# Kernel optimization log

Hardware: AMD Instinct MI355X
Metric: run time of the kernel (lower is better)

## Reference

```python
import jax, jax.numpy as jnp
import numpy as np

B, S, C = 2, 2048, 1024
U, H = 1024, 16
FFH = int(U * 4.0)
NEG = -1e9
EPS = 1e-5


def setup_inputs() -> dict:
    key = jax.random.key(0)
    ks = jax.random.split(key, 16)
    w = lambda k, sh: jax.random.normal(k, sh, dtype=jnp.float32) * 0.02
    return {
        'x': jax.random.normal(ks[0], (B, S, C), dtype=jnp.float32),
        'wq': w(ks[1], (C, U)), 'bq': jnp.zeros((U,), jnp.float32),
        'wk': w(ks[2], (C, U)), 'bk': jnp.zeros((U,), jnp.float32),
        'wv': w(ks[3], (C, U)), 'bv': jnp.zeros((U,), jnp.float32),
        'wf1': w(ks[4], (U, FFH)), 'bf1': jnp.zeros((FFH,), jnp.float32),
        'wf2': w(ks[5], (FFH, U)), 'bf2': jnp.zeros((U,), jnp.float32),
        'ln_g': jnp.ones((S, U), jnp.float32), 'ln_b': jnp.zeros((S, U), jnp.float32),
        'ffln_g': jnp.ones((S, U), jnp.float32), 'ffln_b': jnp.zeros((S, U), jnp.float32),
    }


def _ln2d(x, g, b):
    # LayerNorm over last two dims ([len_ts, units]) as in nn.LayerNorm([S, U])
    m = jnp.mean(x, axis=(-2, -1), keepdims=True)
    v = jnp.mean(jnp.square(x - m), axis=(-2, -1), keepdims=True)
    return (x - m) * jax.lax.rsqrt(v + EPS) * g + b


def reference(x, wq, bq, wk, bk, wv, bv, wf1, bf1, wf2, bf2, ln_g, ln_b, ffln_g, ffln_b):
    dh = U // H
    Q = (x @ wq + bq).reshape(B, S, H, dh)
    K = (x @ wk + bk).reshape(B, S, H, dh)
    V = (x @ wv + bv).reshape(B, S, H, dh)
    scores = jnp.einsum('bqhd,bkhd->bhqk', Q, K) / jnp.sqrt(jnp.float32(dh))
    mask = jnp.tril(jnp.ones((S, S), dtype=bool))  # causal tril buffer
    scores = jnp.where(mask, scores, NEG)
    attn = jax.nn.softmax(scores, axis=-1)
    out = jnp.einsum('bhqk,bkhd->bqhd', attn, V).reshape(B, S, U)
    out = out + x  # residual
    out = _ln2d(out, ln_g, ln_b)
    ff = jax.nn.relu(out @ wf1 + bf1) @ wf2 + bf2
    out = _ln2d(out + ff, ffln_g, ffln_b)
    return out
```

## Files before the change

### kernel.cpp

```cpp
#include <hip/hip_runtime.h>

typedef short s16x8 __attribute__((ext_vector_type(8)));
typedef float f32x4 __attribute__((ext_vector_type(4)));
typedef unsigned short u16x4 __attribute__((ext_vector_type(4)));

#define DEV static __device__ __forceinline__

DEV unsigned short f2bf(float f) {
  union { float f; unsigned u; } v; v.f = f;
  unsigned r = v.u + 0x7FFFu + ((v.u >> 16) & 1u);
  return (unsigned short)(r >> 16);
}
DEV float bf2f(unsigned short u) {
  union { unsigned u; float f; } v; v.u = (unsigned)u << 16; return v.f;
}

#define GLDS16(src, dst) \
  __builtin_amdgcn_global_load_lds((const __attribute__((address_space(1))) void*)(src), \
                                   (__attribute__((address_space(3))) void*)(dst), 16, 0, 0)

#define MFMA(a, b, c) __builtin_amdgcn_mfma_f32_16x16x32_bf16((a), (b), (c), 0, 0, 0)

__global__ __launch_bounds__(256) void k_f32_to_bf16(const float* __restrict__ in,
                                                     unsigned short* __restrict__ out, int n4) {
  int i = blockIdx.x * 256 + threadIdx.x;
  if (i >= n4) return;
  float4 v = ((const float4*)in)[i];
  u16x4 o; o.x = f2bf(v.x); o.y = f2bf(v.y); o.z = f2bf(v.z); o.w = f2bf(v.w);
  ((u16x4*)out)[i] = o;
}

__global__ __launch_bounds__(256) void k_transpose_w(const float* __restrict__ W,
                                                     unsigned short* __restrict__ Wt,
                                                     int K, int N, float scale) {
  __shared__ float t[64][65];
  int k0 = blockIdx.x * 64, n0 = blockIdx.y * 64;
  int tid = threadIdx.x;
#pragma unroll
  for (int i = 0; i < 16; ++i) {
    int idx = tid + i * 256; int r = idx >> 6, c = idx & 63;
    t[r][c] = W[(size_t)(k0 + r) * N + (n0 + c)];
  }
  __syncthreads();
#pragma unroll
  for (int i = 0; i < 16; ++i) {
    int idx = tid + i * 256; int r = idx >> 6, c = idx & 63;
    Wt[(size_t)(n0 + r) * K + (k0 + c)] = f2bf(t[c][r] * scale);
  }
}

__global__ void k_concat3(const float* __restrict__ a, const float* __restrict__ b,
                          const float* __restrict__ c, float* __restrict__ out, int n, float sa) {
  int i = blockIdx.x * 256 + threadIdx.x;
  if (i >= 3 * n) return;
  int j = (i < n) ? i : (i < 2 * n ? i - n : i - 2 * n);
  out[i] = (i < n) ? a[j] * sa : (i < 2 * n ? b[j] : c[j]);
}

template <int MODE>
__global__ __launch_bounds__(512, 2) void k_gemm8(
    const unsigned short* __restrict__ A, int lda,
    const unsigned short* __restrict__ Bt, int ldb,
    const float* __restrict__ bias,
    unsigned short* __restrict__ Cb, float* __restrict__ Cf, int ldc,
    int K, int nnt, size_t zstride) {
  __shared__ __align__(16) unsigned short As[2 * 2 * 8192];
  __shared__ __align__(16) unsigned short Bs[2 * 2 * 8192];
  int nwg = gridDim.x;
  int bid = blockIdx.x;
  int cpx = nwg >> 3;
  int swz = (bid & 7) * cpx + (bid >> 3);
  int mt = swz / nnt, nt = swz % nnt;
  int m0 = mt * 256, n0 = nt * 256;
  int tid = threadIdx.x, w = tid >> 6, l = tid & 63;
  int wm = (w >> 2) * 128, wn = (w & 3) * 64;
  int kb = blockIdx.z * K;

  int sr = tid >> 2;
  int gsrc = (tid & 3) ^ ((sr >> 1) & 3);
  const unsigned short* Ag0 = A + (size_t)(m0 + sr) * lda + kb + gsrc * 8;
  const unsigned short* Ag1 = Ag0 + (size_t)128 * lda;
  const unsigned short* Bg0 = Bt + (size_t)(n0 + sr) * ldb + kb + gsrc * 8;
  const unsigned short* Bg1 = Bg0 + (size_t)128 * ldb;

#define STG_A(t, kh) do { int _c = (t) * 64 + (kh) * 32; int _d = ((((t) & 1) * 2 + (kh)) * 8192); \
    GLDS16(Ag0 + _c, &As[_d + tid * 8]); GLDS16(Ag1 + _c, &As[_d + 4096 + tid * 8]); } while (0)
#define STG_B(t, kh) do { int _c = (t) * 64 + (kh) * 32; int _d = ((((t) & 1) * 2 + (kh)) * 8192); \
    GLDS16(Bg0 + _c, &Bs[_d + tid * 8]); GLDS16(Bg1 + _c, &Bs[_d + 4096 + tid * 8]); } while (0)

  int lswz = (l >> 1) & 3;
  int acol = ((l >> 4) ^ lswz) * 8;
  const unsigned short* Afr = &As[(wm + (l & 15)) * 32 + acol];
  const unsigned short* Bfr = &Bs[(wn + (l & 15)) * 32 + acol];

  f32x4 acc[8][4] = {};
  int nkt = K >> 6;

  STG_A(0, 0); STG_B(0, 0); STG_A(0, 1); STG_B(0, 1); STG_A(1, 0); STG_B(1, 0);
  asm volatile("s_waitcnt vmcnt(4)" ::: "memory");
  __builtin_amdgcn_s_barrier();
  __builtin_amdgcn_sched_barrier(0);

  for (int t = 0; t < nkt; ++t) {
    int cur = t & 1, rem = nkt - t;
    const unsigned short* ab = Afr + cur * 16384;
    const unsigned short* bb = Bfr + cur * 16384;
    s16x8 af[4], bf[4];
    if (t + 1 < nkt) STG_A(t + 1, 1);
#pragma unroll
    for (int nr = 0; nr < 4; ++nr) bf[nr] = *(const s16x8*)(bb + nr * 512);
#pragma unroll
    for (int mr = 0; mr < 4; ++mr) af[mr] = *(const s16x8*)(ab + mr * 512);
    __builtin_amdgcn_s_setprio(1);
#pragma unroll
    for (int mr = 0; mr < 4; ++mr)
#pragma unroll
      for (int nr = 0; nr < 4; ++nr)
        acc[mr][nr] = MFMA(af[mr], bf[nr], acc[mr][nr]);
    __builtin_amdgcn_s_setprio(0);
    if (t + 1 < nkt) STG_B(t + 1, 1);
#pragma unroll
    for (int mr = 0; mr < 4; ++mr) af[mr] = *(const s16x8*)(ab + 2048 + mr * 512);
    __builtin_amdgcn_s_setprio(1);
#pragma unroll
    for (int mr = 0; mr < 4; ++mr)
#pragma unroll
      for (int nr = 0; nr < 4; ++nr)
        acc[mr + 4][nr] = MFMA(af[mr], bf[nr], acc[mr + 4][nr]);
    __builtin_amdgcn_s_setprio(0);
    if (rem >= 2) { asm volatile("s_waitcnt vmcnt(4)" ::: "memory"); }
    else          { asm volatile("s_waitcnt vmcnt(0)" ::: "memory"); }
    __builtin_amdgcn_s_barrier();
    __builtin_amdgcn_sched_barrier(0);
    if (t + 2 < nkt) STG_A(t + 2, 0);
#pragma unroll
    for (int nr = 0; nr < 4; ++nr) bf[nr] = *(const s16x8*)(bb + 8192 + nr * 512);
#pragma unroll
    for (int mr = 0; mr < 4; ++mr) af[mr] = *(const s16x8*)(ab + 8192 + mr * 512);
    __builtin_amdgcn_s_setprio(1);
#pragma unroll
    for (int mr = 0; mr < 4; ++mr)
#pragma unroll
      for (int nr = 0; nr < 4; ++nr)
        acc[mr][nr] = MFMA(af[mr], bf[nr], acc[mr][nr]);
    __builtin_amdgcn_s_setprio(0);
    if (t + 2 < nkt) STG_B(t + 2, 0);
#pragma unroll
    for (int mr = 0; mr < 4; ++mr) af[mr] = *(const s16x8*)(ab + 8192 + 2048 + mr * 512);
    __builtin_amdgcn_s_setprio(1);
#pragma unroll
    for (int mr = 0; mr < 4; ++mr)
#pragma unroll
      for (int nr = 0; nr < 4; ++nr)
        acc[mr + 4][nr] = MFMA(af[mr], bf[nr], acc[mr + 4][nr]);
    __builtin_amdgcn_s_setprio(0);
    if (rem >= 3) { asm volatile("s_waitcnt vmcnt(4)" ::: "memory"); }
    else          { asm volatile("s_waitcnt vmcnt(0)" ::: "memory"); }
    __builtin_amdgcn_s_barrier();
    __builtin_amdgcn_sched_barrier(0);
  }
#undef STG_A
#undef STG_B

  unsigned short* Cbz = (MODE == 3) ? (Cb + zstride * blockIdx.z) : Cb;
#pragma unroll
  for (int mr = 0; mr < 8; ++mr) {
    int rb = m0 + wm + mr * 16 + (l >> 4) * 4;
#pragma unroll
    for (int nr = 0; nr < 4; ++nr) {
      int col = n0 + wn + nr * 16 + (l & 15);
      float bv = (MODE == 3) ? 0.f : bias[col];
#pragma unroll
      for (int j = 0; j < 4; ++j) {
        float v = acc[mr][nr][j] + bv;
        size_t off = (size_t)(rb + j) * ldc + col;
        if (MODE == 1) v = fmaxf(v, 0.f);
        Cbz[off] = f2bf(v);
      }
    }
  }
}

__global__ __launch_bounds__(256) void k_ff2_reduce(
    unsigned short* __restrict__ slices, const float* __restrict__ bias,
    const unsigned short* __restrict__ resid, float* __restrict__ partials) {
  __shared__ float red[8];
  int i = blockIdx.x;
  size_t rb = (size_t)i * 4096;
  int c = threadIdx.x * 4;
  u16x4 a0 = *(const u16x4*)(slices + rb + c);
  u16x4 a1 = *(const u16x4*)(slices + rb + 1024 + c);
  u16x4 a2 = *(const u16x4*)(slices + rb + 2048 + c);
  u16x4 a3 = *(const u16x4*)(slices + rb + 3072 + c);
  float4 bv = *(const float4*)(bias + c);
  u16x4 rv = *(const u16x4*)(resid + (size_t)i * 1024 + c);
  float4 o;
  o.x = bf2f(a0.x) + bf2f(a1.x) + bf2f(a2.x) + bf2f(a3.x) + bv.x + bf2f(rv.x);
  o.y = bf2f(a0.y) + bf2f(a1.y) + bf2f(a2.y) + bf2f(a3.y) + bv.y + bf2f(rv.y);
  o.z = bf2f(a0.z) + bf2f(a1.z) + bf2f(a2.z) + bf2f(a3.z) + bv.z + bf2f(rv.z);
  o.w = bf2f(a0.w) + bf2f(a1.w) + bf2f(a2.w) + bf2f(a3.w) + bv.w + bf2f(rv.w);
  __syncthreads();
  *(float4*)((float*)slices + (size_t)i * 2048 + c) = o;
  float bsum = o.x + o.y + o.z + o.w;
  float bsq = o.x * o.x + o.y * o.y + o.z * o.z + o.w * o.w;
  int wv = threadIdx.x >> 6, lv = threadIdx.x & 63;
#pragma unroll
  for (int mk = 1; mk < 64; mk <<= 1) { bsum += __shfl_xor(bsum, mk); bsq += __shfl_xor(bsq, mk); }
  if (lv == 0) { red[wv] = bsum; red[4 + wv] = bsq; }
  __syncthreads();
  if (threadIdx.x == 0) {
    partials[i * 2] = red[0] + red[1] + red[2] + red[3];
    partials[i * 2 + 1] = red[4] + red[5] + red[6] + red[7];
  }
}

__global__ __launch_bounds__(256) void k_transpose_v(const unsigned short* __restrict__ V, int ldv,
                                                     unsigned short* __restrict__ Vt, int S, int H) {
  __shared__ __align__(16) unsigned short t[64][72];
  int s0 = blockIdx.x * 64;
  int bh = blockIdx.y; int b = bh / H, h = bh % H;
  const unsigned short* src = V + (size_t)(b * S) * ldv + h * 64;
  unsigned short* dst = Vt + (size_t)bh * 64 * S;
  int tid = threadIdx.x;
#pragma unroll
  for (int i = 0; i < 2; ++i) {
    int idx = tid + i * 256;
    int s = idx >> 3, c = (idx & 7) * 8;
    s16x8 v = *(const s16x8*)(src + (size_t)(s0 + s) * ldv + c);
#pragma unroll
    for (int j = 0; j < 8; ++j) t[c + j][s] = (unsigned short)v[j];
  }
  __syncthreads();
#pragma unroll
  for (int i = 0; i < 2; ++i) {
    int idx = tid + i * 256;
    int d = idx >> 3, c = (idx & 7) * 8;
    *(s16x8*)(dst + (size_t)d * S + s0 + c) = *(const s16x8*)&t[d][c];
  }
}

__global__ __launch_bounds__(256) void k_attn(
    const unsigned short* __restrict__ Qg, const unsigned short* __restrict__ Kg,
    const unsigned short* __restrict__ Vt, int ldqk,
    const float* __restrict__ x, float* __restrict__ hpre,
    float* __restrict__ partials, int S, int H) {
  __shared__ __align__(16) unsigned short Ks[2][64 * 64];
  __shared__ __align__(16) unsigned short Vs[2][64 * 64];
  __shared__ __align__(16) unsigned short Ps[4][16 * 64];
  __shared__ float red[8];
  int bh = blockIdx.x, b = bh >> 4, h = bh & 15;
  const int nqt = S / 64;
  int qt = nqt - 1 - (int)blockIdx.y;
  int tid = threadIdx.x, w = tid >> 6, l = tid & 63;
  const int U = H * 64;
  const unsigned short* Qb = Qg + (size_t)(b * S) * ldqk + h * 64;
  const unsigned short* Kb = Kg + (size_t)(b * S) * ldqk + h * 64;
  const unsigned short* Vb = Vt + (size_t)bh * 64 * S;
  const float* xb = x + (size_t)(b * S) * U + h * 64;
  float* hb = hpre + (size_t)(b * S) * U + h * 64;
  int sg_r[2], sg_c[2];
#pragma unroll
  for (int it = 0; it < 2; ++it) {
    int g = it * 256 + tid;
    sg_r[it] = g >> 3;
    sg_c[it] = ((g & 7) ^ ((g >> 3) & 7)) * 8;
  }
  unsigned short* Pw = &Ps[w][0];
  int qloc = l & 15;
  int kloc = (l >> 4) * 4;

  int qrow = qt * 64 + w * 16 + qloc;
  s16x8 qf0 = *(const s16x8*)(Qb + (size_t)qrow * ldqk + (l >> 4) * 8);
  s16x8 qf1 = *(const s16x8*)(Qb + (size_t)qrow * ldqk + 32 + (l >> 4) * 8);
  f32x4 o[4] = {};
  float m = -1e30f, lsum = 0.f;

#pragma unroll
  for (int it = 0; it < 2; ++it) {
    GLDS16(Kb + (size_t)sg_r[it] * ldqk + sg_c[it], &Ks[0][(it * 256 + tid) * 8]);
    GLDS16(Vb + (size_t)sg_r[it] * S + sg_c[it], &Vs[0][(it * 256 + tid) * 8]);
  }

  for (int kt = 0; kt <= qt; ++kt) {
    int cur = kt & 1;
    __syncthreads();
    if (kt < qt) {
      int nb = cur ^ 1, kn = (kt + 1) * 64;
#pragma unroll
      for (int it = 0; it < 2; ++it) {
        GLDS16(Kb + (size_t)(kn + sg_r[it]) * ldqk + sg_c[it], &Ks[nb][(it * 256 + tid) * 8]);
        GLDS16(Vb + (size_t)sg_r[it] * S + kn + sg_c[it], &Vs[nb][(it * 256 + tid) * 8]);
      }
    }
    f32x4 sc[4];
    __builtin_amdgcn_s_setprio(1);
#pragma unroll
    for (int fn = 0; fn < 4; ++fn) {
      int row = fn * 16 + (l & 15);
      s16x8 kf0 = *(const s16x8*)&Ks[cur][row * 64 + ((((l >> 4)) ^ (row & 7)) * 8)];
      s16x8 kf1 = *(const s16x8*)&Ks[cur][row * 64 + (((4 + (l >> 4)) ^ (row & 7)) * 8)];
      f32x4 z = {};
      z = MFMA(kf0, qf0, z);
      z = MFMA(kf1, qf1, z);
      sc[fn] = z;
    }
    __builtin_amdgcn_s_setprio(0);
    if (kt == qt) {
      int qsel = w * 16 + qloc;
#pragma unroll
      for (int fn = 0; fn < 4; ++fn)
#pragma unroll
        for (int j = 0; j < 4; ++j)
          if (fn * 16 + kloc + j > qsel) sc[fn][j] = -1e30f;
    }
    float mx = sc[0][0];
#pragma unroll
    for (int fn = 0; fn < 4; ++fn)
#pragma unroll
      for (int j = 0; j < 4; ++j) mx = fmaxf(mx, sc[fn][j]);
    mx = fmaxf(mx, __shfl_xor(mx, 16));
    mx = fmaxf(mx, __shfl_xor(mx, 32));
    if (__ballot(mx > m + 8.f)) {
      float mnew = fmaxf(m, mx);
      float alpha = __expf(m - mnew);
      m = mnew;
      lsum *= alpha;
#pragma unroll
      for (int j = 0; j < 4; ++j) {
        float aj = __shfl(alpha, (l & 48) | (kloc + j));
#pragma unroll
        for (int fd = 0; fd < 4; ++fd) o[fd][j] *= aj;
      }
    }
    float rs = 0.f;
#pragma unroll
    for (int fn = 0; fn < 4; ++fn) {
      u16x4 pk;
#pragma unroll
      for (int j = 0; j < 4; ++j) {
        float p = __expf(sc[fn][j] - m);
        rs += p;
        ((unsigned short*)&pk)[j] = f2bf(p);
      }
      int kb2 = fn * 16 + kloc;
      int el = qloc * 64 + (((kb2 >> 3) ^ (qloc & 7)) * 8) + (kb2 & 7);
      *(u16x4*)&Pw[el] = pk;
    }
    rs += __shfl_xor(rs, 16);
    rs += __shfl_xor(rs, 32);
    lsum += rs;
    __builtin_amdgcn_s_setprio(1);
#pragma unroll
    for (int kk = 0; kk < 2; ++kk) {
      int prow = l & 15;
      s16x8 pa = *(const s16x8*)&Pw[prow * 64 + (((kk * 4 + (l >> 4)) ^ (prow & 7)) * 8)];
#pragma unroll
      for (int fd = 0; fd < 4; ++fd) {
        int vrow = fd * 16 + (l & 15);
        s16x8 vf = *(const s16x8*)&Vs[cur][vrow * 64 + (((kk * 4 + (l >> 4)) ^ (vrow & 7)) * 8)];
        o[fd] = MFMA(pa, vf, o[fd]);
      }
    }
    __builtin_amdgcn_s_setprio(0);
  }
  float bsum = 0.f, bsq = 0.f;
#pragma unroll
  for (int j = 0; j < 4; ++j) {
    float lr = __shfl(lsum, (l & 48) | (kloc + j));
    float inv = 1.f / lr;
    int row = qt * 64 + w * 16 + kloc + j;
#pragma unroll
    for (int fd = 0; fd < 4; ++fd) {
      int col = fd * 16 + (l & 15);
      float v = o[fd][j] * inv + xb[(size_t)row * U + col];
      hb[(size_t)row * U + col] = v;
      bsum += v; bsq += v * v;
    }
  }
#pragma unroll
  for (int mk = 1; mk < 64; mk <<= 1) { bsum += __shfl_xor(bsum, mk); bsq += __shfl_xor(bsq, mk); }
  if (l == 0) { red[w] = bsum; red[4 + w] = bsq; }
  __syncthreads();
  if (tid == 0) {
    float s2 = red[0] + red[1] + red[2] + red[3];
    float q2 = red[4] + red[5] + red[6] + red[7];
    int pi = b * (H * nqt) + h * nqt + qt;
    partials[pi * 2] = s2; partials[pi * 2 + 1] = q2;
  }
}

__global__ __launch_bounds__(256) void k_ln_stats(const float* __restrict__ partials, int nper,
                                                  float* __restrict__ stats, float invN) {
  int b = blockIdx.x, tid = threadIdx.x;
  float s = 0.f, q = 0.f;
  for (int i = tid; i < nper; i += 256) { s += partials[(b * nper + i) * 2]; q += partials[(b * nper + i) * 2 + 1]; }
#pragma unroll
  for (int mk = 1; mk < 64; mk <<= 1) { s += __shfl_xor(s, mk); q += __shfl_xor(q, mk); }
  __shared__ float red[8];
  int w = tid >> 6, l = tid & 63;
  if (l == 0) { red[w] = s; red[4 + w] = q; }
  __syncthreads();
  if (tid == 0) {
    s = red[0] + red[1] + red[2] + red[3];
    q = red[4] + red[5] + red[6] + red[7];
    float m = s * invN, var = q * invN - m * m;
    stats[b * 2] = m; stats[b * 2 + 1] = rsqrtf(var + 1e-5f);
  }
}

__global__ __launch_bounds__(256) void k_ln_apply(
    const float* __restrict__ src, const float* __restrict__ stats,
    const float* __restrict__ g, const float* __restrict__ bt,
    float* __restrict__ outf, unsigned short* __restrict__ outb, int SU) {
  int b = blockIdx.y;
  int idx = (blockIdx.x * 256 + threadIdx.x) * 4;
  float m = stats[b * 2], r = stats[b * 2 + 1];
  float4 v = *(const float4*)(src + (size_t)b * SU + idx);
  float4 gg = *(const float4*)(g + idx);
  float4 bb = *(const float4*)(bt + idx);
  float4 o;
  o.x = (v.x - m) * r * gg.x + bb.x;
  o.y = (v.y - m) * r * gg.y + bb.y;
  o.z = (v.z - m) * r * gg.z + bb.z;
  o.w = (v.w - m) * r * gg.w + bb.w;
  if (outf) *(float4*)(outf + (size_t)b * SU + idx) = o;
  if (outb) {
    u16x4 ob; ob.x = f2bf(o.x); ob.y = f2bf(o.y); ob.z = f2bf(o.z); ob.w = f2bf(o.w);
    *(u16x4*)(outb + (size_t)b * SU + idx) = ob;
  }
}

__global__ __launch_bounds__(256) void k_ln_apply2(
    const float* __restrict__ src, const float* __restrict__ stats,
    const float* __restrict__ g, const float* __restrict__ bt,
    float* __restrict__ outf) {
  int b = blockIdx.y;
  int row = blockIdx.x;
  int grow = b * 2048 + row;
  int c = threadIdx.x * 4;
  float m = stats[b * 2], r = stats[b * 2 + 1];
  float4 v = *(const float4*)(src + (size_t)grow * 2048 + c);
  float4 gg = *(const float4*)(g + (size_t)row * 1024 + c);
  float4 bb = *(const float4*)(bt + (size_t)row * 1024 + c);
  float4 o;
  o.x = (v.x - m) * r * gg.x + bb.x;
  o.y = (v.y - m) * r * gg.y + bb.y;
  o.z = (v.z - m) * r * gg.z + bb.z;
  o.w = (v.w - m) * r * gg.w + bb.w;
  *(float4*)(outf + (size_t)grow * 1024 + c) = o;
}

extern "C" void kernel_launch(void* const* d_in, const int* in_sizes, int n_in,
                              void* d_out, int out_size, void* d_ws, size_t ws_size,
                              hipStream_t stream) {
  (void)in_sizes; (void)n_in; (void)out_size; (void)ws_size;
  const int S = 2048, H = 16;
  const float* x   = (const float*)d_in[0];
  const float* wq  = (const float*)d_in[1];
  const float* bq  = (const float*)d_in[2];
  const float* wk  = (const float*)d_in[3];
  const float* bk  = (const float*)d_in[4];
  const float* wv  = (const float*)d_in[5];
  const float* bv  = (const float*)d_in[6];
  const float* wf1 = (const float*)d_in[7];
  const float* bf1 = (const float*)d_in[8];
  const float* wf2 = (const float*)d_in[9];
  const float* bf2 = (const float*)d_in[10];
  const float* lng = (const float*)d_in[11];
  const float* lnb = (const float*)d_in[12];
  const float* ffg = (const float*)d_in[13];
  const float* ffb = (const float*)d_in[14];

  char* ws = (char*)d_ws;
  unsigned short* wqkvT = (unsigned short*)(ws);
  unsigned short* wf1T  = (unsigned short*)(ws + 6291456);
  unsigned short* wf2T  = (unsigned short*)(ws + 14680064);
  unsigned short* xb    = (unsigned short*)(ws + 23068672);
  unsigned short* qkv   = (unsigned short*)(ws + 31457280);
  unsigned short* vt    = (unsigned short*)(ws + 56623104);
  unsigned short* h1b   = (unsigned short*)(ws + 65011712);
  float* hpre           = (float*)(ws + 73400320);
  unsigned short* ff2s  = (unsigned short*)(ws + 73400320);
  unsigned short* f1b   = (unsigned short*)(ws + 23068672);
  float* biasqkv        = (float*)(ws + 106954752);
  float* part_attn      = (float*)(ws + 106967040);
  float* stats1         = (float*)(ws + 106977280);
  float* ffpart2        = (float*)(ws);
  float* stats2         = (float*)(ws + 65536);

  k_f32_to_bf16<<<4096, 256, 0, stream>>>(x, xb, 4096 * 1024 / 4);
  k_transpose_w<<<dim3(16, 16), 256, 0, stream>>>(wq, wqkvT, 1024, 1024, 0.125f);
  k_transpose_w<<<dim3(16, 16), 256, 0, stream>>>(wk, wqkvT + 1024 * 1024, 1024, 1024, 1.0f);
  k_transpose_w<<<dim3(16, 16), 256, 0, stream>>>(wv, wqkvT + 2048 * 1024, 1024, 1024, 1.0f);
  k_transpose_w<<<dim3(16, 64), 256, 0, stream>>>(wf1, wf1T, 1024, 4096, 1.0f);
  k_transpose_w<<<dim3(64, 16), 256, 0, stream>>>(wf2, wf2T, 4096, 1024, 1.0f);
  k_concat3<<<12, 256, 0, stream>>>(bq, bk, bv, biasqkv, 1024, 0.125f);

  k_gemm8<0><<<dim3(192, 1, 1), 512, 0, stream>>>(xb, 1024, wqkvT, 1024, biasqkv,
      qkv, nullptr, 3072, 1024, 12, 0);

  k_transpose_v<<<dim3(32, 32), 256, 0, stream>>>(qkv + 2048, 3072, vt, S, H);

  k_attn<<<dim3(32, 32), 256, 0, stream>>>(qkv, qkv + 1024, vt, 3072, x, hpre, part_attn, S, H);

  k_ln_stats<<<2, 256, 0, stream>>>(part_attn, 512, stats1, 1.f / (2048.f * 1024.f));
  k_ln_apply<<<dim3(2048, 2), 256, 0, stream>>>(hpre, stats1, lng, lnb, nullptr, h1b, S * 1024);

  k_gemm8<1><<<dim3(256, 1, 1), 512, 0, stream>>>(h1b, 1024, wf1T, 1024, bf1,
      f1b, nullptr, 4096, 1024, 16, 0);

  k_gemm8<3><<<dim3(64, 1, 4), 512, 0, stream>>>(f1b, 4096, wf2T, 4096, nullptr,
      ff2s, nullptr, 4096, 1024, 4, 1024);

  k_ff2_reduce<<<4096, 256, 0, stream>>>(ff2s, bf2, h1b, ffpart2);

  k_ln_stats<<<2, 256, 0, stream>>>(ffpart2, 2048, stats2, 1.f / (2048.f * 1024.f));
  k_ln_apply2<<<dim3(2048, 2), 256, 0, stream>>>((float*)ff2s, stats2, ffg, ffb, (float*)d_out);
}
```

Before: 237.2 us.

## Store pre-LN attention output in bf16 and use exp2 softmax with prescaled Q

Attention now writes the residual-added pre-LayerNorm activations as bf16 instead of fp32, and the LN apply kernel reads bf16, which halves that intermediate's traffic. The Q weights and bias are prescaled by log2(e), so the softmax uses exp2f and the rescale threshold is adjusted to match. f2bf now uses the HIP intrinsic, and the reduction scratch reuses the P shared buffer. The price is extra rounding error in the activations that feed the first LayerNorm.

```diff
diff --git a/kernel.cpp b/kernel.cpp
--- a/kernel.cpp
+++ b/kernel.cpp
@@ -1,4 +1,5 @@
 #include <hip/hip_runtime.h>
+#include <hip/hip_bf16.h>
 
 typedef short s16x8 __attribute__((ext_vector_type(8)));
 typedef float f32x4 __attribute__((ext_vector_type(4)));
@@ -7,9 +8,8 @@
 #define DEV static __device__ __forceinline__
 
 DEV unsigned short f2bf(float f) {
-  union { float f; unsigned u; } v; v.f = f;
-  unsigned r = v.u + 0x7FFFu + ((v.u >> 16) & 1u);
-  return (unsigned short)(r >> 16);
+  __hip_bfloat16 h = __float2bfloat16(f);
+  return *reinterpret_cast<unsigned short*>(&h);
 }
 DEV float bf2f(unsigned short u) {
   union { unsigned u; float f; } v; v.u = (unsigned)u << 16; return v.f;
@@ -242,12 +242,11 @@
 __global__ __launch_bounds__(256) void k_attn(
     const unsigned short* __restrict__ Qg, const unsigned short* __restrict__ Kg,
     const unsigned short* __restrict__ Vt, int ldqk,
-    const float* __restrict__ x, float* __restrict__ hpre,
+    const float* __restrict__ x, unsigned short* __restrict__ hpre,
     float* __restrict__ partials, int S, int H) {
   __shared__ __align__(16) unsigned short Ks[2][64 * 64];
   __shared__ __align__(16) unsigned short Vs[2][64 * 64];
   __shared__ __align__(16) unsigned short Ps[4][16 * 64];
-  __shared__ float red[8];
   int bh = blockIdx.x, b = bh >> 4, h = bh & 15;
   const int nqt = S / 64;
   int qt = nqt - 1 - (int)blockIdx.y;
@@ -257,7 +256,7 @@
   const unsigned short* Kb = Kg + (size_t)(b * S) * ldqk + h * 64;
   const unsigned short* Vb = Vt + (size_t)bh * 64 * S;
   const float* xb = x + (size_t)(b * S) * U + h * 64;
-  float* hb = hpre + (size_t)(b * S) * U + h * 64;
+  unsigned short* hb = hpre + (size_t)(b * S) * U + h * 64;
   int sg_r[2], sg_c[2];
 #pragma unroll
   for (int it = 0; it < 2; ++it) {
@@ -320,9 +319,9 @@
       for (int j = 0; j < 4; ++j) mx = fmaxf(mx, sc[fn][j]);
     mx = fmaxf(mx, __shfl_xor(mx, 16));
     mx = fmaxf(mx, __shfl_xor(mx, 32));
-    if (__ballot(mx > m + 8.f)) {
+    if (__ballot(mx > m + 11.5415603f)) {
       float mnew = fmaxf(m, mx);
-      float alpha = __expf(m - mnew);
+      float alpha = exp2f(m - mnew);
       m = mnew;
       lsum *= alpha;
 #pragma unroll
@@ -338,7 +337,7 @@
       u16x4 pk;
 #pragma unroll
       for (int j = 0; j < 4; ++j) {
-        float p = __expf(sc[fn][j] - m);
+        float p = exp2f(sc[fn][j] - m);
         rs += p;
         ((unsigned short*)&pk)[j] = f2bf(p);
       }
@@ -373,17 +372,18 @@
     for (int fd = 0; fd < 4; ++fd) {
       int col = fd * 16 + (l & 15);
       float v = o[fd][j] * inv + xb[(size_t)row * U + col];
-      hb[(size_t)row * U + col] = v;
+      hb[(size_t)row * U + col] = f2bf(v);
       bsum += v; bsq += v * v;
     }
   }
 #pragma unroll
   for (int mk = 1; mk < 64; mk <<= 1) { bsum += __shfl_xor(bsum, mk); bsq += __shfl_xor(bsq, mk); }
-  if (l == 0) { red[w] = bsum; red[4 + w] = bsq; }
+  if (l == 0) { float* r = (float*)&Ps[w][0]; r[0] = bsum; r[1] = bsq; }
   __syncthreads();
   if (tid == 0) {
-    float s2 = red[0] + red[1] + red[2] + red[3];
-    float q2 = red[4] + red[5] + red[6] + red[7];
+    float s2 = 0.f, q2 = 0.f;
+#pragma unroll
+    for (int ww = 0; ww < 4; ++ww) { const float* r = (const float*)&Ps[ww][0]; s2 += r[0]; q2 += r[1]; }
     int pi = b * (H * nqt) + h * nqt + qt;
     partials[pi * 2] = s2; partials[pi * 2 + 1] = q2;
   }
@@ -408,26 +408,22 @@
   }
 }
 
-__global__ __launch_bounds__(256) void k_ln_apply(
-    const float* __restrict__ src, const float* __restrict__ stats,
+__global__ __launch_bounds__(256) void k_ln_apply_b(
+    const unsigned short* __restrict__ src, const float* __restrict__ stats,
     const float* __restrict__ g, const float* __restrict__ bt,
-    float* __restrict__ outf, unsigned short* __restrict__ outb, int SU) {
+    unsigned short* __restrict__ outb, int SU) {
   int b = blockIdx.y;
   int idx = (blockIdx.x * 256 + threadIdx.x) * 4;
   float m = stats[b * 2], r = stats[b * 2 + 1];
-  float4 v = *(const float4*)(src + (size_t)b * SU + idx);
+  u16x4 v4 = *(const u16x4*)(src + (size_t)b * SU + idx);
   float4 gg = *(const float4*)(g + idx);
   float4 bb = *(const float4*)(bt + idx);
-  float4 o;
-  o.x = (v.x - m) * r * gg.x + bb.x;
-  o.y = (v.y - m) * r * gg.y + bb.y;
-  o.z = (v.z - m) * r * gg.z + bb.z;
-  o.w = (v.w - m) * r * gg.w + bb.w;
-  if (outf) *(float4*)(outf + (size_t)b * SU + idx) = o;
-  if (outb) {
-    u16x4 ob; ob.x = f2bf(o.x); ob.y = f2bf(o.y); ob.z = f2bf(o.z); ob.w = f2bf(o.w);
-    *(u16x4*)(outb + (size_t)b * SU + idx) = ob;
-  }
+  u16x4 ob;
+  ob.x = f2bf((bf2f(v4.x) - m) * r * gg.x + bb.x);
+  ob.y = f2bf((bf2f(v4.y) - m) * r * gg.y + bb.y);
+  ob.z = f2bf((bf2f(v4.z) - m) * r * gg.z + bb.z);
+  ob.w = f2bf((bf2f(v4.w) - m) * r * gg.w + bb.w);
+  *(u16x4*)(outb + (size_t)b * SU + idx) = ob;
 }
 
 __global__ __launch_bounds__(256) void k_ln_apply2(
@@ -479,7 +475,7 @@
   unsigned short* qkv   = (unsigned short*)(ws + 31457280);
   unsigned short* vt    = (unsigned short*)(ws + 56623104);
   unsigned short* h1b   = (unsigned short*)(ws + 65011712);
-  float* hpre           = (float*)(ws + 73400320);
+  unsigned short* hpreb = (unsigned short*)(ws + 73400320);
   unsigned short* ff2s  = (unsigned short*)(ws + 73400320);
   unsigned short* f1b   = (unsigned short*)(ws + 23068672);
   float* biasqkv        = (float*)(ws + 106954752);
@@ -488,23 +484,24 @@
   float* ffpart2        = (float*)(ws);
   float* stats2         = (float*)(ws + 65536);
 
+  const float qscale = 0.125f * 1.44269504f;
   k_f32_to_bf16<<<4096, 256, 0, stream>>>(x, xb, 4096 * 1024 / 4);
-  k_transpose_w<<<dim3(16, 16), 256, 0, stream>>>(wq, wqkvT, 1024, 1024, 0.125f);
+  k_transpose_w<<<dim3(16, 16), 256, 0, stream>>>(wq, wqkvT, 1024, 1024, qscale);
   k_transpose_w<<<dim3(16, 16), 256, 0, stream>>>(wk, wqkvT + 1024 * 1024, 1024, 1024, 1.0f);
   k_transpose_w<<<dim3(16, 16), 256, 0, stream>>>(wv, wqkvT + 2048 * 1024, 1024, 1024, 1.0f);
   k_transpose_w<<<dim3(16, 64), 256, 0, stream>>>(wf1, wf1T, 1024, 4096, 1.0f);
   k_transpose_w<<<dim3(64, 16), 256, 0, stream>>>(wf2, wf2T, 4096, 1024, 1.0f);
-  k_concat3<<<12, 256, 0, stream>>>(bq, bk, bv, biasqkv, 1024, 0.125f);
+  k_concat3<<<12, 256, 0, stream>>>(bq, bk, bv, biasqkv, 1024, qscale);
 
   k_gemm8<0><<<dim3(192, 1, 1), 512, 0, stream>>>(xb, 1024, wqkvT, 1024, biasqkv,
       qkv, nullptr, 3072, 1024, 12, 0);
 
   k_transpose_v<<<dim3(32, 32), 256, 0, stream>>>(qkv + 2048, 3072, vt, S, H);
 
-  k_attn<<<dim3(32, 32), 256, 0, stream>>>(qkv, qkv + 1024, vt, 3072, x, hpre, part_attn, S, H);
+  k_attn<<<dim3(32, 32), 256, 0, stream>>>(qkv, qkv + 1024, vt, 3072, x, hpreb, part_attn, S, H);
 
   k_ln_stats<<<2, 256, 0, stream>>>(part_attn, 512, stats1, 1.f / (2048.f * 1024.f));
-  k_ln_apply<<<dim3(2048, 2), 256, 0, stream>>>(hpre, stats1, lng, lnb, nullptr, h1b, S * 1024);
+  k_ln_apply_b<<<dim3(2048, 2), 256, 0, stream>>>(hpreb, stats1, lng, lnb, h1b, S * 1024);
 
   k_gemm8<1><<<dim3(256, 1, 1), 512, 0, stream>>>(h1b, 1024, wf1T, 1024, bf1,
       f1b, nullptr, 4096, 1024, 16, 0);
```

Result: no change. 236.2 us (-0.4%).
